# Kernel tuning notes

Hardware: AMD Instinct MI355X
Metric: run time of the kernel (lower is better)

## Reference

```python
import jax, jax.numpy as jnp
import numpy as np

H = 8      # n_heads
DK = 64    # d_k per head
EPS = 1e-5       # InstanceNorm1d eps
SLOPE = 0.01     # LeakyReLU negative slope


def setup_inputs() -> dict:
    key = jax.random.key(0)
    ks = jax.random.split(key, 6)
    B, C, L = 16, 256, 1024
    HD = H * DK  # 512
    return {
        "x": jax.random.normal(ks[0], (B, C, L), dtype=jnp.float32),
        "Wq": jax.random.normal(ks[1], (HD, C), dtype=jnp.float32) * 0.02,
        "Wk": jax.random.normal(ks[2], (HD, C), dtype=jnp.float32) * 0.02,
        "Wv": jax.random.normal(ks[3], (HD, C), dtype=jnp.float32) * 0.02,
        "Wo": jax.random.normal(ks[4], (C, HD), dtype=jnp.float32) * 0.02,
        "gamma": jax.random.normal(ks[5], (1,), dtype=jnp.float32),
    }


def reference(x, Wq, Wk, Wv, Wo, gamma):
    B, C, L = x.shape
    # conv1x1 projections (bias=False) == channel matmuls -> [B, H*DK, L]
    # then reshape/permute into heads: [B, H, L, DK]
    def proj(W):
        y = jnp.einsum('oc,bcl->bol', W, x)          # [B, H*DK, L]
        return y.reshape(B, H, DK, L).transpose(0, 1, 3, 2)  # [B, H, L, DK]

    q, k, v = proj(Wq), proj(Wk), proj(Wv)
    # softmax-free linear attention: (Q K^T / d_k) V
    logits = jnp.einsum('bhld,bhmd->bhlm', q, k) / DK  # [B, H, L, L]
    out = jnp.einsum('bhlm,bhmd->bhld', logits, v)     # [B, H, L, DK]
    # merge heads back to channel-first [B, H*DK, L]
    merged = out.transpose(0, 1, 3, 2).reshape(B, H * DK, L)
    # output conv1x1 -> [B, C, L]
    o = jnp.einsum('oc,bcl->bol', Wo, merged)
    # InstanceNorm1d (affine=False): normalize over L per (b, c)
    mu = jnp.mean(o, axis=-1, keepdims=True)
    var = jnp.var(o, axis=-1, keepdims=True)
    o = (o - mu) * jax.lax.rsqrt(var + EPS)
    # gamma-scaled residual + LeakyReLU
    y = o * gamma + x
    return jnp.where(y >= 0, y, SLOPE * y)
```

## Files before the change

kernel.cpp:

```cpp
#include <hip/hip_runtime.h>

typedef __bf16 bf16;
typedef bf16 bf16x8 __attribute__((ext_vector_type(8)));
typedef bf16 bf16x4 __attribute__((ext_vector_type(4)));
typedef float f32x4 __attribute__((ext_vector_type(4)));

#define EPS 1e-5f
#define SLOPE 0.01f

__device__ __forceinline__ void gld_lds16(const bf16* g, bf16* l) {
    __builtin_amdgcn_global_load_lds(
        (const __attribute__((address_space(1))) unsigned int*)g,
        (__attribute__((address_space(3))) unsigned int*)l, 16, 0, 0);
}

__global__ __launch_bounds__(256) void prep_kernel(
    const float* __restrict__ x,
    const float* __restrict__ Wq, const float* __restrict__ Wk,
    const float* __restrict__ Wv, const float* __restrict__ Wo,
    bf16* __restrict__ xT, bf16* __restrict__ xB,
    bf16* __restrict__ WkB, bf16* __restrict__ WvB,
    bf16* __restrict__ WoB, bf16* __restrict__ WqT)
{
    __shared__ float tile[64][65];
    const int id = blockIdx.x;
    const int t = threadIdx.x;
    if (id < 1024) {
        const int lt = id & 15, ct = (id >> 4) & 3, b = id >> 6;
        {
            const int cl = t >> 2;
            const int l4 = (t & 3) << 4;
            const float* src = x + (size_t)(b * 256 + ct * 64 + cl) * 1024 + lt * 64 + l4;
            float4 v0 = ((const float4*)src)[0];
            float4 v1 = ((const float4*)src)[1];
            float4 v2 = ((const float4*)src)[2];
            float4 v3 = ((const float4*)src)[3];
            bf16x8 r0, r1;
            r0[0]=(bf16)v0.x; r0[1]=(bf16)v0.y; r0[2]=(bf16)v0.z; r0[3]=(bf16)v0.w;
            r0[4]=(bf16)v1.x; r0[5]=(bf16)v1.y; r0[6]=(bf16)v1.z; r0[7]=(bf16)v1.w;
            r1[0]=(bf16)v2.x; r1[1]=(bf16)v2.y; r1[2]=(bf16)v2.z; r1[3]=(bf16)v2.w;
            r1[4]=(bf16)v3.x; r1[5]=(bf16)v3.y; r1[6]=(bf16)v3.z; r1[7]=(bf16)v3.w;
            bf16* xbd = xB + (size_t)(b * 256 + ct * 64 + cl) * 1024 + lt * 64 + l4;
            *(bf16x8*)xbd = r0;
            *(bf16x8*)(xbd + 8) = r1;
            float* tr = &tile[cl][l4];
            tr[0]=v0.x; tr[1]=v0.y; tr[2]=v0.z; tr[3]=v0.w;
            tr[4]=v1.x; tr[5]=v1.y; tr[6]=v1.z; tr[7]=v1.w;
            tr[8]=v2.x; tr[9]=v2.y; tr[10]=v2.z; tr[11]=v2.w;
            tr[12]=v3.x; tr[13]=v3.y; tr[14]=v3.z; tr[15]=v3.w;
        }
        __syncthreads();
        {
            const int lw = t >> 2;
            const int ec = (t & 3) << 4;
            bf16x8 o0, o1;
            #pragma unroll
            for (int ii = 0; ii < 8; ++ii) {
                o0[ii] = (bf16)tile[ec + ii][lw];
                o1[ii] = (bf16)tile[ec + 8 + ii][lw];
            }
            bf16* dst = xT + (size_t)(b * 1024 + lt * 64 + lw) * 256 + ct * 64 + ec;
            *(bf16x8*)dst = o0;
            *(bf16x8*)(dst + 8) = o1;
        }
    } else if (id < 1408) {
        const int i = (id - 1024) * 1024 + t * 4;
        const float* src; bf16* dst;
        if (i < 131072)      { src = Wk + i;            dst = WkB + i; }
        else if (i < 262144) { src = Wv + (i - 131072); dst = WvB + (i - 131072); }
        else                 { src = Wo + (i - 262144); dst = WoB + (i - 262144); }
        float4 v = *(const float4*)src;
        bf16x4 o;
        o[0]=(bf16)v.x; o[1]=(bf16)v.y; o[2]=(bf16)v.z; o[3]=(bf16)v.w;
        *(bf16x4*)dst = o;
    } else {
        const int id2 = id - 1408;
        const int h = id2 >> 2, ct = id2 & 3;
        {
            const int e  = t >> 2;
            const int c4 = (t & 3) << 4;
            const float* src = Wq + (size_t)(h * 64 + e) * 256 + ct * 64 + c4;
            float4 v0 = ((const float4*)src)[0];
            float4 v1 = ((const float4*)src)[1];
            float4 v2 = ((const float4*)src)[2];
            float4 v3 = ((const float4*)src)[3];
            float* tr = &tile[e][c4];
            tr[0]=v0.x; tr[1]=v0.y; tr[2]=v0.z; tr[3]=v0.w;
            tr[4]=v1.x; tr[5]=v1.y; tr[6]=v1.z; tr[7]=v1.w;
            tr[8]=v2.x; tr[9]=v2.y; tr[10]=v2.z; tr[11]=v2.w;
            tr[12]=v3.x; tr[13]=v3.y; tr[14]=v3.z; tr[15]=v3.w;
        }
        __syncthreads();
        {
            const int c  = t >> 2;
            const int e4 = (t & 3) << 4;
            bf16x8 o0, o1;
            #pragma unroll
            for (int ii = 0; ii < 8; ++ii) {
                o0[ii] = (bf16)tile[e4 + ii][c];
                o1[ii] = (bf16)tile[e4 + 8 + ii][c];
            }
            bf16* dst = WqT + (size_t)h * 16384 + (size_t)(ct * 64 + c) * 64 + e4;
            *(bf16x8*)dst = o0;
            *(bf16x8*)(dst + 8) = o1;
        }
    }
}

template<int KDIM, typename OutT>
__global__ __launch_bounds__(256) void gemm128_bt(
    const bf16* __restrict__ A, const bf16* __restrict__ Bt, OutT* __restrict__ C,
    long long sA, long long sBt, long long sC, int ldC)
{
    __shared__ bf16 As[128 * 32];
    __shared__ bf16 Bs[128 * 32];
    const int z = blockIdx.z;
    A  += (size_t)z * sA;
    Bt += (size_t)z * sBt;
    C  += (size_t)z * sC;
    const int m0 = blockIdx.x * 128;
    const int n0 = blockIdx.y * 128;
    const int t = threadIdx.x, w = t >> 6, l = t & 63;
    const int srow = w * 16 + (l >> 2);
    const int ske  = (l & 3) * 8;
    const bf16* ga = A  + (size_t)(m0 + srow) * KDIM + ske;
    const bf16* gb = Bt + (size_t)(n0 + srow) * KDIM + ske;
    bf16* la = As + srow * 32 + ske;
    bf16* lb = Bs + srow * 32 + ske;
    const int lm = l & 15, lq = l >> 4;
    const int wm = (w & 1) * 64, wn = (w >> 1) * 64;

    f32x4 acc[4][4] = {};
    for (int kt = 0; kt < KDIM / 32; ++kt) {
        const int k0 = kt * 32;
        gld_lds16(ga + k0, la);
        gld_lds16(ga + k0 + (size_t)64 * KDIM, la + 64 * 32);
        gld_lds16(gb + k0, lb);
        gld_lds16(gb + k0 + (size_t)64 * KDIM, lb + 64 * 32);
        __syncthreads();
        bf16x8 af[4], bfr[4];
        #pragma unroll
        for (int i = 0; i < 4; ++i)
            af[i] = *(const bf16x8*)(As + (wm + i * 16 + lm) * 32 + lq * 8);
        #pragma unroll
        for (int j = 0; j < 4; ++j)
            bfr[j] = *(const bf16x8*)(Bs + (wn + j * 16 + lm) * 32 + lq * 8);
        #pragma unroll
        for (int i = 0; i < 4; ++i)
            #pragma unroll
            for (int j = 0; j < 4; ++j)
                acc[i][j] = __builtin_amdgcn_mfma_f32_16x16x32_bf16(af[i], bfr[j], acc[i][j], 0, 0, 0);
        __syncthreads();
    }
    #pragma unroll
    for (int i = 0; i < 4; ++i)
        #pragma unroll
        for (int j = 0; j < 4; ++j) {
            const int row = m0 + wm + i * 16 + lq * 4;
            const int col = n0 + wn + j * 16 + lm;
            OutT* cp = C + (size_t)row * ldC + col;
            #pragma unroll
            for (int r = 0; r < 4; ++r)
                cp[(size_t)r * ldC] = (OutT)acc[i][j][r];
        }
}

__global__ __launch_bounds__(256) void tm_kernel(
    const bf16* __restrict__ S, const bf16* __restrict__ WkB,
    const bf16* __restrict__ WqT, bf16* __restrict__ WmT)
{
    __shared__ __align__(16) bf16 regA[16384];
    __shared__ __align__(16) bf16 Qb[16384];
    bf16* Sc = regA;
    bf16* Kc = regA + 8192;
    bf16* Tb = regA;

    const int bh = blockIdx.x;
    const int b = bh >> 3, h = bh & 7;
    const bf16* Sg = S   + (size_t)b * 131072 + (size_t)h * 64 * 256;
    const bf16* Kg = WkB + (size_t)h * 64 * 256;
    const bf16* Qg = WqT + (size_t)h * 16384;
    const int t = threadIdx.x, w = t >> 6, l = t & 63;
    const int lm = l & 15, lq = l >> 4;

    #pragma unroll
    for (int it = 0; it < 8; ++it) {
        const int idx = it * 256 + t;
        const int r = idx >> 3, s = idx & 7;
        gld_lds16(Qg + (size_t)r * 64 + (s ^ (r & 7)) * 8, Qb + r * 64 + s * 8);
    }

    f32x4 accT[4] = {};
    for (int ck = 0; ck < 2; ++ck) {
        const int k0 = ck * 128;
        #pragma unroll
        for (int it = 0; it < 4; ++it) {
            const int idx = it * 256 + t;
            const int r = idx >> 4, s = idx & 15;
            const int gs = (s ^ (r & 7)) * 8;
            gld_lds16(Sg + (size_t)r * 256 + k0 + gs, Sc + r * 128 + s * 8);
            gld_lds16(Kg + (size_t)r * 256 + k0 + gs, Kc + r * 128 + s * 8);
        }
        __syncthreads();
        #pragma unroll
        for (int ks = 0; ks < 4; ++ks) {
            const int q = ks * 4 + lq;
            const int ra = w * 16 + lm;
            bf16x8 a = *(const bf16x8*)(Sc + ra * 128 + (q ^ (ra & 7)) * 8);
            #pragma unroll
            for (int nf = 0; nf < 4; ++nf) {
                const int rb = nf * 16 + lm;
                bf16x8 bb = *(const bf16x8*)(Kc + rb * 128 + (q ^ (rb & 7)) * 8);
                accT[nf] = __builtin_amdgcn_mfma_f32_16x16x32_bf16(a, bb, accT[nf], 0, 0, 0);
            }
        }
        __syncthreads();
    }
    #pragma unroll
    for (int nf = 0; nf < 4; ++nf)
        #pragma unroll
        for (int ri = 0; ri < 4; ++ri) {
            const int row = w * 16 + lq * 4 + ri;
            const int col = nf * 16 + lm;
            Tb[row * 64 + (((col >> 3) ^ (row & 7)) << 3) + (col & 7)] =
                (bf16)(accT[nf][ri] * 0.015625f);
        }
    __syncthreads();

    f32x4 accM[4][4] = {};
    #pragma unroll
    for (int ks = 0; ks < 2; ++ks) {
        const int q = ks * 4 + lq;
        bf16x8 bfrag[4];
        #pragma unroll
        for (int nf = 0; nf < 4; ++nf) {
            const int rb = nf * 16 + lm;
            bfrag[nf] = *(const bf16x8*)(Tb + rb * 64 + (q ^ (rb & 7)) * 8);
        }
        #pragma unroll
        for (int mf = 0; mf < 4; ++mf) {
            const int ra = w * 64 + mf * 16 + lm;
            bf16x8 a = *(const bf16x8*)(Qb + ra * 64 + (q ^ (ra & 7)) * 8);
            #pragma unroll
            for (int nf = 0; nf < 4; ++nf)
                accM[mf][nf] = __builtin_amdgcn_mfma_f32_16x16x32_bf16(a, bfrag[nf], accM[mf][nf], 0, 0, 0);
        }
    }
    bf16* Wg = WmT + (size_t)b * 131072 + h * 64;
    #pragma unroll
    for (int mf = 0; mf < 4; ++mf)
        #pragma unroll
        for (int nf = 0; nf < 4; ++nf)
            #pragma unroll
            for (int ri = 0; ri < 4; ++ri) {
                const int c = w * 64 + mf * 16 + lq * 4 + ri;
                const int d = nf * 16 + lm;
                Wg[(size_t)c * 512 + d] = (bf16)accM[mf][nf][ri];
            }
}

__global__ __launch_bounds__(256) void norm_kernel(
    const bf16* __restrict__ o, const bf16* __restrict__ xB,
    const float* __restrict__ gamma, float* __restrict__ y)
{
    const size_t row = blockIdx.x;
    const bf16* orow = o + row * 1024;
    const bf16* xrow = xB + row * 1024;
    float* yrow = y + row * 1024;
    const int tid = threadIdx.x;

    bf16x4 ov = *(const bf16x4*)(orow + tid * 4);
    float4 v = {(float)ov[0], (float)ov[1], (float)ov[2], (float)ov[3]};
    float s  = v.x + v.y + v.z + v.w;
    float ss = v.x * v.x + v.y * v.y + v.z * v.z + v.w * v.w;
    #pragma unroll
    for (int off = 32; off > 0; off >>= 1) {
        s  += __shfl_down(s, off);
        ss += __shfl_down(ss, off);
    }
    __shared__ float red[10];
    const int wave = tid >> 6, lane = tid & 63;
    if (lane == 0) { red[wave] = s; red[4 + wave] = ss; }
    __syncthreads();
    if (tid == 0) {
        float a  = red[0] + red[1] + red[2] + red[3];
        float b2 = red[4] + red[5] + red[6] + red[7];
        float mu = a * (1.0f / 1024.0f);
        float var = b2 * (1.0f / 1024.0f) - mu * mu;
        red[8] = mu;
        red[9] = rsqrtf(var + EPS);
    }
    __syncthreads();
    const float mu = red[8], inv = red[9], g = gamma[0];
    bf16x4 xv4 = *(const bf16x4*)(xrow + tid * 4);
    float4 r;
    r.x = (v.x - mu) * inv * g + (float)xv4[0];
    r.y = (v.y - mu) * inv * g + (float)xv4[1];
    r.z = (v.z - mu) * inv * g + (float)xv4[2];
    r.w = (v.w - mu) * inv * g + (float)xv4[3];
    r.x = r.x >= 0.f ? r.x : SLOPE * r.x;
    r.y = r.y >= 0.f ? r.y : SLOPE * r.y;
    r.z = r.z >= 0.f ? r.z : SLOPE * r.z;
    r.w = r.w >= 0.f ? r.w : SLOPE * r.w;
    ((float4*)yrow)[tid] = r;
}

extern "C" void kernel_launch(void* const* d_in, const int* in_sizes, int n_in,
                              void* d_out, int out_size, void* d_ws, size_t ws_size,
                              hipStream_t stream) {
    const float* x     = (const float*)d_in[0];
    const float* Wq    = (const float*)d_in[1];
    const float* Wk    = (const float*)d_in[2];
    const float* Wv    = (const float*)d_in[3];
    const float* Wo    = (const float*)d_in[4];
    const float* gamma = (const float*)d_in[5];
    float* y = (float*)d_out;

    char* wsb = (char*)d_ws;
    bf16* xT  = (bf16*)(wsb);
    bf16* xB  = (bf16*)(wsb +  8388608);
    bf16* WkB = (bf16*)(wsb + 16777216);
    bf16* WvB = (bf16*)(wsb + 17039360);
    bf16* WoB = (bf16*)(wsb + 17301504);
    bf16* WqT = (bf16*)(wsb + 17563648);
    bf16* G   = (bf16*)(wsb + 17825792);
    bf16* S   = (bf16*)(wsb + 19922944);
    bf16* WmT = (bf16*)(wsb + 24117248);
    bf16* Wt  = (bf16*)(wsb + 28311552);
    bf16* o   = (bf16*)(wsb + 30408704);

    prep_kernel<<<dim3(1440), 256, 0, stream>>>(x, Wq, Wk, Wv, Wo, xT, xB, WkB, WvB, WoB, WqT);

    gemm128_bt<1024, bf16><<<dim3(2, 2, 16), 256, 0, stream>>>(
        xB, xB, G, 262144LL, 262144LL, 65536LL, 256);

    gemm128_bt<256, bf16><<<dim3(4, 2, 16), 256, 0, stream>>>(
        WvB, G, S, 0LL, 65536LL, 131072LL, 256);

    tm_kernel<<<dim3(128), 256, 0, stream>>>(S, WkB, WqT, WmT);

    gemm128_bt<512, bf16><<<dim3(2, 2, 16), 256, 0, stream>>>(
        WoB, WmT, Wt, 0LL, 131072LL, 65536LL, 256);

    gemm128_bt<256, bf16><<<dim3(2, 8, 16), 256, 0, stream>>>(
        Wt, xT, o, 65536LL, 262144LL, 262144LL, 1024);

    norm_kernel<<<dim3(4096), 256, 0, stream>>>(o, xB, gamma, y);
}
```

Measured before the change: 138.8 us.

## Multi-stage async LDS pipelining in gemm128_bt and tm_kernel loads

The GEMM kernel gets a 5-stage ring of shared-memory buffers. Global-to-LDS loads are issued several k-tiles ahead, and explicit vmcnt waits replace the two __syncthreads per iteration with a single barrier. The tm_kernel now keeps separate double buffers for both S/K chunks and issues all of its loads up front, so the second chunk's transfer overlaps the first chunk's MFMAs. This raises LDS usage, which may lower occupancy, and correctness depends on the hand-coded waitcnt counts matching the number of outstanding loads.

```diff
diff --git a/kernel.cpp b/kernel.cpp
--- a/kernel.cpp
+++ b/kernel.cpp
@@ -112,8 +112,10 @@
     const bf16* __restrict__ A, const bf16* __restrict__ Bt, OutT* __restrict__ C,
     long long sA, long long sBt, long long sC, int ldC)
 {
-    __shared__ bf16 As[128 * 32];
-    __shared__ bf16 Bs[128 * 32];
+    constexpr int NT = KDIM / 32;
+    constexpr int NB = 5;
+    __shared__ bf16 As[NB][128 * 32];
+    __shared__ bf16 Bs[NB][128 * 32];
     const int z = blockIdx.z;
     A  += (size_t)z * sA;
     Bt += (size_t)z * sBt;
@@ -125,32 +127,55 @@
     const int ske  = (l & 3) * 8;
     const bf16* ga = A  + (size_t)(m0 + srow) * KDIM + ske;
     const bf16* gb = Bt + (size_t)(n0 + srow) * KDIM + ske;
-    bf16* la = As + srow * 32 + ske;
-    bf16* lb = Bs + srow * 32 + ske;
+    const int loff = srow * 32 + ske;
     const int lm = l & 15, lq = l >> 4;
     const int wm = (w & 1) * 64, wn = (w >> 1) * 64;
 
+    #pragma unroll
+    for (int i = 0; i < NB - 1; ++i) {
+        const int k0 = i * 32;
+        gld_lds16(ga + k0, &As[i][0] + loff);
+        gld_lds16(ga + k0 + (size_t)64 * KDIM, &As[i][0] + 64 * 32 + loff);
+        gld_lds16(gb + k0, &Bs[i][0] + loff);
+        gld_lds16(gb + k0 + (size_t)64 * KDIM, &Bs[i][0] + 64 * 32 + loff);
+    }
+
     f32x4 acc[4][4] = {};
-    for (int kt = 0; kt < KDIM / 32; ++kt) {
-        const int k0 = kt * 32;
-        gld_lds16(ga + k0, la);
-        gld_lds16(ga + k0 + (size_t)64 * KDIM, la + 64 * 32);
-        gld_lds16(gb + k0, lb);
-        gld_lds16(gb + k0 + (size_t)64 * KDIM, lb + 64 * 32);
-        __syncthreads();
+    int cur = 0, stg = NB - 1;
+    for (int kt = 0; kt < NT; ++kt) {
+        const int remain = NT - 1 - kt;
+        if (remain >= 3)      asm volatile("s_waitcnt vmcnt(12)" ::: "memory");
+        else if (remain == 2) asm volatile("s_waitcnt vmcnt(8)"  ::: "memory");
+        else if (remain == 1) asm volatile("s_waitcnt vmcnt(4)"  ::: "memory");
+        else                  asm volatile("s_waitcnt vmcnt(0)"  ::: "memory");
+        __builtin_amdgcn_s_barrier();
+        __builtin_amdgcn_sched_barrier(0);
+        const int kst = kt + NB - 1;
+        if (kst < NT) {
+            const int k0 = kst * 32;
+            bf16* la = &As[stg][0] + loff;
+            bf16* lb = &Bs[stg][0] + loff;
+            gld_lds16(ga + k0, la);
+            gld_lds16(ga + k0 + (size_t)64 * KDIM, la + 64 * 32);
+            gld_lds16(gb + k0, lb);
+            gld_lds16(gb + k0 + (size_t)64 * KDIM, lb + 64 * 32);
+        }
+        const bf16* Ab = &As[cur][0];
+        const bf16* Bb = &Bs[cur][0];
         bf16x8 af[4], bfr[4];
         #pragma unroll
         for (int i = 0; i < 4; ++i)
-            af[i] = *(const bf16x8*)(As + (wm + i * 16 + lm) * 32 + lq * 8);
+            af[i] = *(const bf16x8*)(Ab + (wm + i * 16 + lm) * 32 + lq * 8);
         #pragma unroll
         for (int j = 0; j < 4; ++j)
-            bfr[j] = *(const bf16x8*)(Bs + (wn + j * 16 + lm) * 32 + lq * 8);
+            bfr[j] = *(const bf16x8*)(Bb + (wn + j * 16 + lm) * 32 + lq * 8);
         #pragma unroll
         for (int i = 0; i < 4; ++i)
             #pragma unroll
             for (int j = 0; j < 4; ++j)
                 acc[i][j] = __builtin_amdgcn_mfma_f32_16x16x32_bf16(af[i], bfr[j], acc[i][j], 0, 0, 0);
-        __syncthreads();
+        cur = (cur + 1 == NB) ? 0 : cur + 1;
+        stg = (stg + 1 == NB) ? 0 : stg + 1;
     }
     #pragma unroll
     for (int i = 0; i < 4; ++i)
@@ -169,11 +194,10 @@
     const bf16* __restrict__ S, const bf16* __restrict__ WkB,
     const bf16* __restrict__ WqT, bf16* __restrict__ WmT)
 {
-    __shared__ __align__(16) bf16 regA[16384];
+    __shared__ __align__(16) bf16 Sc[2][8192];
+    __shared__ __align__(16) bf16 Kc[2][8192];
     __shared__ __align__(16) bf16 Qb[16384];
-    bf16* Sc = regA;
-    bf16* Kc = regA + 8192;
-    bf16* Tb = regA;
+    __shared__ __align__(16) bf16 Tb[4096];
 
     const int bh = blockIdx.x;
     const int b = bh >> 3, h = bh & 7;
@@ -184,37 +208,58 @@
     const int lm = l & 15, lq = l >> 4;
 
     #pragma unroll
+    for (int it = 0; it < 4; ++it) {
+        const int idx = it * 256 + t;
+        const int r = idx >> 4, s2 = idx & 15;
+        const int gs = (s2 ^ (r & 7)) * 8;
+        gld_lds16(Sg + (size_t)r * 256 + gs, &Sc[0][0] + r * 128 + s2 * 8);
+        gld_lds16(Kg + (size_t)r * 256 + gs, &Kc[0][0] + r * 128 + s2 * 8);
+    }
+    #pragma unroll
     for (int it = 0; it < 8; ++it) {
         const int idx = it * 256 + t;
-        const int r = idx >> 3, s = idx & 7;
-        gld_lds16(Qg + (size_t)r * 64 + (s ^ (r & 7)) * 8, Qb + r * 64 + s * 8);
+        const int r = idx >> 3, s2 = idx & 7;
+        gld_lds16(Qg + (size_t)r * 64 + (s2 ^ (r & 7)) * 8, Qb + r * 64 + s2 * 8);
+    }
+    #pragma unroll
+    for (int it = 0; it < 4; ++it) {
+        const int idx = it * 256 + t;
+        const int r = idx >> 4, s2 = idx & 15;
+        const int gs = (s2 ^ (r & 7)) * 8;
+        gld_lds16(Sg + (size_t)r * 256 + 128 + gs, &Sc[1][0] + r * 128 + s2 * 8);
+        gld_lds16(Kg + (size_t)r * 256 + 128 + gs, &Kc[1][0] + r * 128 + s2 * 8);
     }
 
     f32x4 accT[4] = {};
-    for (int ck = 0; ck < 2; ++ck) {
-        const int k0 = ck * 128;
-        #pragma unroll
-        for (int it = 0; it < 4; ++it) {
-            const int idx = it * 256 + t;
-            const int r = idx >> 4, s = idx & 15;
-            const int gs = (s ^ (r & 7)) * 8;
-            gld_lds16(Sg + (size_t)r * 256 + k0 + gs, Sc + r * 128 + s * 8);
-            gld_lds16(Kg + (size_t)r * 256 + k0 + gs, Kc + r * 128 + s * 8);
-        }
-        __syncthreads();
-        #pragma unroll
-        for (int ks = 0; ks < 4; ++ks) {
-            const int q = ks * 4 + lq;
-            const int ra = w * 16 + lm;
-            bf16x8 a = *(const bf16x8*)(Sc + ra * 128 + (q ^ (ra & 7)) * 8);
-            #pragma unroll
-            for (int nf = 0; nf < 4; ++nf) {
-                const int rb = nf * 16 + lm;
-                bf16x8 bb = *(const bf16x8*)(Kc + rb * 128 + (q ^ (rb & 7)) * 8);
-                accT[nf] = __builtin_amdgcn_mfma_f32_16x16x32_bf16(a, bb, accT[nf], 0, 0, 0);
-            }
-        }
-        __syncthreads();
+    asm volatile("s_waitcnt vmcnt(16)" ::: "memory");
+    __builtin_amdgcn_s_barrier();
+    __builtin_amdgcn_sched_barrier(0);
+    #pragma unroll
+    for (int ks = 0; ks < 4; ++ks) {
+        const int q = ks * 4 + lq;
+        const int ra = w * 16 + lm;
+        bf16x8 a = *(const bf16x8*)(&Sc[0][0] + ra * 128 + (q ^ (ra & 7)) * 8);
+        #pragma unroll
+        for (int nf = 0; nf < 4; ++nf) {
+            const int rb = nf * 16 + lm;
+            bf16x8 bb = *(const bf16x8*)(&Kc[0][0] + rb * 128 + (q ^ (rb & 7)) * 8);
+            accT[nf] = __builtin_amdgcn_mfma_f32_16x16x32_bf16(a, bb, accT[nf], 0, 0, 0);
+        }
+    }
+    asm volatile("s_waitcnt vmcnt(0)" ::: "memory");
+    __builtin_amdgcn_s_barrier();
+    __builtin_amdgcn_sched_barrier(0);
+    #pragma unroll
+    for (int ks = 0; ks < 4; ++ks) {
+        const int q = ks * 4 + lq;
+        const int ra = w * 16 + lm;
+        bf16x8 a = *(const bf16x8*)(&Sc[1][0] + ra * 128 + (q ^ (ra & 7)) * 8);
+        #pragma unroll
+        for (int nf = 0; nf < 4; ++nf) {
+            const int rb = nf * 16 + lm;
+            bf16x8 bb = *(const bf16x8*)(&Kc[1][0] + rb * 128 + (q ^ (rb & 7)) * 8);
+            accT[nf] = __builtin_amdgcn_mfma_f32_16x16x32_bf16(a, bb, accT[nf], 0, 0, 0);
+        }
     }
     #pragma unroll
     for (int nf = 0; nf < 4; ++nf)
```

Result: no change. 139.1 us (+0.3%).
